# Kernel optimization log

Hardware: AMD Instinct MI355X
Metric: run time of the kernel (lower is better)

The kernel has to match this reference:

```python
import jax, jax.numpy as jnp
import numpy as np

HEADS = 4
DIM_HEAD = 32
SCALE = 16.0
EPS = 1e-5  # jax.nn.standardize default


def _standardize(t):
    # standardize over last axis (the flattened x*y*z sequence), per (b, h, d)
    mu = jnp.mean(t, axis=-1, keepdims=True)
    var = jnp.var(t, axis=-1, keepdims=True)
    return (t - mu) * jax.lax.rsqrt(var + EPS)


def setup_inputs() -> dict:
    key = jax.random.key(0)
    k1, k2, k3 = jax.random.split(key, 3)
    dim = 64
    hidden = HEADS * DIM_HEAD  # 128
    b, x, y, z = 2, 16, 16, 16
    inp = jax.random.normal(k1, (b, x, y, z, dim), dtype=jnp.float32)
    # 1x1x1 convs == pointwise channel matmuls; init like flax lecun_normal-ish scale
    w_qkv = jax.random.normal(k2, (dim, 3 * hidden), dtype=jnp.float32) / np.sqrt(dim)
    w_out = jax.random.normal(k3, (hidden, dim), dtype=jnp.float32) / np.sqrt(hidden)
    b_out = jnp.zeros((dim,), dtype=jnp.float32)
    return {"input": inp, "w_qkv": w_qkv, "w_out": w_out, "b_out": b_out}


def reference(input, w_qkv, w_out, b_out):
    b, x, y, z, c = input.shape
    s = x * y * z
    # pointwise conv -> qkv
    qkv = jnp.einsum('bxyzc,cd->bxyzd', input, w_qkv)  # [b,x,y,z,3*hidden]
    q, k, v = jnp.split(qkv, 3, axis=-1)
    # rearrange 'b x y z (h c) -> b h c (x y z)'
    def to_bhds(t):
        return t.reshape(b, s, HEADS, DIM_HEAD).transpose(0, 2, 3, 1)  # [b,h,d,s]
    q, k, v = map(to_bhds, (q, k, v))
    q = _standardize(q)
    k = _standardize(k)
    sim = jnp.einsum('bhdi,bhdj->bhij', q, k) * SCALE  # [b,h,s,s]
    attn = jax.nn.softmax(sim, axis=-1)
    out = jnp.einsum('bhij,bhdj->bhid', attn, v)  # [b,h,s,d]
    # rearrange 'b h (x y z) d -> b x y z (h d)'
    out = out.transpose(0, 2, 1, 3).reshape(b, x, y, z, HEADS * DIM_HEAD)
    return jnp.einsum('bxyzc,co->bxyzo', out, w_out) + b_out
```

## Files before the change

### kernel.cpp

```cpp
#include <hip/hip_runtime.h>
#include <math.h>
#include <stdint.h>


typedef __attribute__((ext_vector_type(8))) short short8;
typedef __attribute__((ext_vector_type(4))) float f32x4;
typedef __attribute__((ext_vector_type(16))) float f32x16;

#define QSCALE 23.083120654223414f

#if __has_builtin(__builtin_amdgcn_exp2f)
#define EXP2F(x) __builtin_amdgcn_exp2f(x)
#else
#define EXP2F(x) exp2f(x)
#endif

__device__ inline uint32_t pack_hilo(float y) {
  uint32_t uy = __float_as_uint(y);
  uint32_t hb = (uy + 0x7fffu + ((uy >> 16) & 1u)) >> 16;
  float hf = __uint_as_float(hb << 16);
  float r = y - hf;
  uint32_t ur = __float_as_uint(r);
  uint32_t lb = (ur + 0x7fffu + ((ur >> 16) & 1u)) >> 16;
  return (hb << 16) | (lb & 0xffffu);
}

__device__ inline ushort f32_to_bf16(float y) {
  uint32_t uy = __float_as_uint(y);
  return (ushort)((uy + 0x7fffu + ((uy >> 16) & 1u)) >> 16);
}

__device__ inline float bpermf(int addr, float v) {
  return __int_as_float(__builtin_amdgcn_ds_bpermute(addr, __float_as_int(v)));
}

__global__ __launch_bounds__(256) void qkv_kernel(const float* __restrict__ in,
                                                  const float* __restrict__ w,
                                                  float* __restrict__ qf,
                                                  float* __restrict__ kf,
                                                  ushort* __restrict__ vhg,
                                                  float* __restrict__ psum,
                                                  float* __restrict__ psq) {
  __shared__ float As[64][68];
  __shared__ float Bs[64][68];
  __shared__ float ssum[64], ssq[64];
  const int ctile = blockIdx.x % 6;
  const int stile = blockIdx.x / 6;
  const int tid = threadIdx.x;
  const int row0 = stile * 64;
  const int sel = ctile >> 1;

  if (tid < 64) { ssum[tid] = 0.f; ssq[tid] = 0.f; }
  for (int idx = tid; idx < 64 * 64; idx += 256) {
    int s = idx >> 6, c = idx & 63;
    As[s][c] = in[(size_t)(row0 + s) * 64 + c];
  }
  for (int idx = tid; idx < 64 * 64; idx += 256) {
    int c = idx >> 6, ch = idx & 63;
    Bs[c][ch] = w[(size_t)c * 384 + ctile * 64 + ch];
  }
  __syncthreads();

  const int ts = tid >> 4, tc = tid & 15;
  float acc[4][4] = {};
  for (int c = 0; c < 64; c += 4) {
    float4 av[4];
#pragma unroll
    for (int a = 0; a < 4; ++a) av[a] = *(const float4*)&As[ts * 4 + a][c];
    const float4 b0 = *(const float4*)&Bs[c + 0][tc * 4];
    const float4 b1 = *(const float4*)&Bs[c + 1][tc * 4];
    const float4 b2 = *(const float4*)&Bs[c + 2][tc * 4];
    const float4 b3 = *(const float4*)&Bs[c + 3][tc * 4];
    const float bm[4][4] = {{b0.x, b0.y, b0.z, b0.w},
                            {b1.x, b1.y, b1.z, b1.w},
                            {b2.x, b2.y, b2.z, b2.w},
                            {b3.x, b3.y, b3.z, b3.w}};
#pragma unroll
    for (int a = 0; a < 4; ++a) {
      const float aw[4] = {av[a].x, av[a].y, av[a].z, av[a].w};
#pragma unroll
      for (int j = 0; j < 4; ++j)
#pragma unroll
        for (int cc = 0; cc < 4; ++cc) acc[a][cc] = fmaf(aw[j], bm[j][cc], acc[a][cc]);
    }
  }

  const int b = row0 >> 12;
  const int sl = (row0 & 4095) + ts * 4;
  const int chg0 = ctile * 64 + tc * 4;

  if (sel < 2) {
    const int hd0 = chg0 & 127;
    const int h = hd0 >> 5, d0 = hd0 & 31;
    float* dst = (sel == 0 ? qf : kf) + ((size_t)(b * 4 + h) * 4096) * 32 + d0;
#pragma unroll
    for (int a = 0; a < 4; ++a) {
      float4 st = make_float4(acc[a][0], acc[a][1], acc[a][2], acc[a][3]);
      *(float4*)&dst[(size_t)(sl + a) * 32] = st;
    }
#pragma unroll
    for (int cc = 0; cc < 4; ++cc) {
      float sm = acc[0][cc] + acc[1][cc] + acc[2][cc] + acc[3][cc];
      float sq = acc[0][cc] * acc[0][cc] + acc[1][cc] * acc[1][cc] +
                 acc[2][cc] * acc[2][cc] + acc[3][cc] * acc[3][cc];
      atomicAdd(&ssum[tc * 4 + cc], sm);
      atomicAdd(&ssq[tc * 4 + cc], sq);
    }
    __syncthreads();
    if (tid < 64) {
      const int ch = (ctile & 1) * 64 + tid;
      const int idx = (((sel * 2 + b) * 128) + ch) * 64 + (stile & 63);
      psum[idx] = ssum[tid];
      psq[idx] = ssq[tid];
    }
  } else {
    __syncthreads();
    float* VT = &As[0][0];
#pragma unroll
    for (int cc = 0; cc < 4; ++cc)
      *(float4*)&VT[(tc * 4 + cc) * 68 + ts * 4] =
          make_float4(acc[0][cc], acc[1][cc], acc[2][cc], acc[3][cc]);
    __syncthreads();
#pragma unroll
    for (int t2 = 0; t2 < 2; ++t2) {
      const int lin = tid + t2 * 256;
      const int ch = lin >> 3, gg = lin & 7;
      const float4 f0 = *(const float4*)&VT[ch * 68 + gg * 8];
      const float4 f1 = *(const float4*)&VT[ch * 68 + gg * 8 + 4];
      uint4 pk;
      pk.x = (uint32_t)f32_to_bf16(f0.x) | ((uint32_t)f32_to_bf16(f0.y) << 16);
      pk.y = (uint32_t)f32_to_bf16(f0.z) | ((uint32_t)f32_to_bf16(f0.w) << 16);
      pk.z = (uint32_t)f32_to_bf16(f1.x) | ((uint32_t)f32_to_bf16(f1.y) << 16);
      pk.w = (uint32_t)f32_to_bf16(f1.z) | ((uint32_t)f32_to_bf16(f1.w) << 16);
      const int hd = (ctile * 64 + ch) & 127;
      const int h = hd >> 5, d = hd & 31;
      *(uint4*)&vhg[((size_t)(b * 4 + h) * 32 + d) * 4096 + (row0 & 4095) + gg * 8] = pk;
    }
  }
}

__global__ __launch_bounds__(256) void norm_kernel(const float* __restrict__ kf,
                                                   ushort* __restrict__ khg,
                                                   ushort* __restrict__ klg,
                                                   const float* __restrict__ psum,
                                                   const float* __restrict__ psq,
                                                   float* __restrict__ qA,
                                                   float* __restrict__ qB) {
  const int bx = blockIdx.x;
  const int tid = threadIdx.x;
  if (bx == 128) {
    const int base = (((tid >> 7) * 128) + (tid & 127)) * 64;
    float sm = 0.f, sq = 0.f;
#pragma unroll 8
    for (int e = 0; e < 64; ++e) {
      sm += psum[base + e];
      sq += psq[base + e];
    }
    const float mu = sm * (1.f / 4096.f);
    const float inv = rsqrtf(sq * (1.f / 4096.f) - mu * mu + 1e-5f) * QSCALE;
    qA[tid] = inv;
    qB[tid] = -mu * inv;
    return;
  }
  __shared__ float red[2][32][8];
  __shared__ float kA[32], kB[32];
  const int bh = bx >> 4;
  const int s0 = (bx & 15) * 256;
  {
    const int d = tid >> 3, p = tid & 7;
    const int base = ((2 + (bh >> 2)) * 128 + (bh & 3) * 32 + d) * 64 + p * 8;
    float sm = 0.f, sq = 0.f;
#pragma unroll
    for (int e = 0; e < 8; ++e) {
      sm += psum[base + e];
      sq += psq[base + e];
    }
    red[0][d][p] = sm;
    red[1][d][p] = sq;
  }
  __syncthreads();
  if (tid < 32) {
    float sm = 0.f, sq = 0.f;
#pragma unroll
    for (int e = 0; e < 8; ++e) {
      sm += red[0][tid][e];
      sq += red[1][tid][e];
    }
    const float mu = sm * (1.f / 4096.f);
    const float inv = rsqrtf(sq * (1.f / 4096.f) - mu * mu + 1e-5f);
    kA[tid] = inv;
    kB[tid] = -mu * inv;
  }
  __syncthreads();

  const int d0 = (tid & 7) * 4;
  const float A0 = kA[d0], A1 = kA[d0 + 1], A2 = kA[d0 + 2], A3 = kA[d0 + 3];
  const float B0 = kB[d0], B1 = kB[d0 + 1], B2 = kB[d0 + 2], B3 = kB[d0 + 3];
  const float* src = kf + ((size_t)bh * 4096 + s0) * 32;
  ushort* dh = khg + ((size_t)bh * 4096 + s0) * 32 + d0;
  ushort* dl = klg + ((size_t)bh * 4096 + s0) * 32 + d0;
#pragma unroll
  for (int i = 0; i < 8; ++i) {
    const int s = (tid + i * 256) >> 3;
    float4 x = *(const float4*)&src[(size_t)s * 32 + d0];
    float y[4] = {fmaf(x.x, A0, B0), fmaf(x.y, A1, B1), fmaf(x.z, A2, B2), fmaf(x.w, A3, B3)};
    ushort4 hi, lo;
    ushort* hp = (ushort*)&hi;
    ushort* lp = (ushort*)&lo;
#pragma unroll
    for (int e = 0; e < 4; ++e) {
      uint32_t pk = pack_hilo(y[e]);
      hp[e] = (ushort)(pk >> 16);
      lp[e] = (ushort)(pk & 0xffff);
    }
    *(ushort4*)&dh[(size_t)s * 32] = hi;
    *(ushort4*)&dl[(size_t)s * 32] = lo;
  }
}

__global__ __launch_bounds__(512, 4) void attn_kernel(const float* __restrict__ qf,
                                                      const float* __restrict__ qA,
                                                      const float* __restrict__ qB,
                                                      const ushort* __restrict__ khg,
                                                      const ushort* __restrict__ klg,
                                                      const ushort* __restrict__ vhg,
                                                      float* __restrict__ o) {
  __shared__ char lds[49152];

  const int tid = threadIdx.x;
  const int strm = tid >> 7;
  const int st = tid & 127;
  const int wv = (tid >> 6) & 1;
  const int lane = tid & 63;
  const int pl = lane & 31;
  const int h2 = lane >> 5;
  const int bh = blockIdx.x >> 6;
  const int i0 = (blockIdx.x & 63) * 64;

  ushort* KHI = (ushort*)lds + strm * 6144;

  const int irow = i0 + wv * 32 + pl;
  const float* qptr = qf + ((size_t)bh * 4096 + irow) * 32;
  short8 qh0, ql0, qh1, ql1;
  {
    const int da = 8 * h2, db = 16 + 8 * h2;
    const float4 x0 = *(const float4*)(qptr + da);
    const float4 x1 = *(const float4*)(qptr + da + 4);
    const float4 x2 = *(const float4*)(qptr + db);
    const float4 x3 = *(const float4*)(qptr + db + 4);
    const float4 A0 = *(const float4*)&qA[bh * 32 + da];
    const float4 A1 = *(const float4*)&qA[bh * 32 + da + 4];
    const float4 A2 = *(const float4*)&qA[bh * 32 + db];
    const float4 A3 = *(const float4*)&qA[bh * 32 + db + 4];
    const float4 B0 = *(const float4*)&qB[bh * 32 + da];
    const float4 B1 = *(const float4*)&qB[bh * 32 + da + 4];
    const float4 B2 = *(const float4*)&qB[bh * 32 + db];
    const float4 B3 = *(const float4*)&qB[bh * 32 + db + 4];
    const float y0[8] = {fmaf(x0.x, A0.x, B0.x), fmaf(x0.y, A0.y, B0.y),
                         fmaf(x0.z, A0.z, B0.z), fmaf(x0.w, A0.w, B0.w),
                         fmaf(x1.x, A1.x, B1.x), fmaf(x1.y, A1.y, B1.y),
                         fmaf(x1.z, A1.z, B1.z), fmaf(x1.w, A1.w, B1.w)};
    const float y1[8] = {fmaf(x2.x, A2.x, B2.x), fmaf(x2.y, A2.y, B2.y),
                         fmaf(x2.z, A2.z, B2.z), fmaf(x2.w, A2.w, B2.w),
                         fmaf(x3.x, A3.x, B3.x), fmaf(x3.y, A3.y, B3.y),
                         fmaf(x3.z, A3.z, B3.z), fmaf(x3.w, A3.w, B3.w)};
#pragma unroll
    for (int j = 0; j < 8; ++j) {
      uint32_t p0 = pack_hilo(y0[j]);
      uint32_t p1 = pack_hilo(y1[j]);
      qh0[j] = (short)(p0 >> 16); ql0[j] = (short)(p0 & 0xffff);
      qh1[j] = (short)(p1 >> 16); ql1[j] = (short)(p1 & 0xffff);
    }
  }

  const int bp32 = (lane ^ 32) << 2;

  const int jr = st >> 2, ck = st & 3;
  const int et = jr >> 4, eh = (jr >> 3) & 1, ee = jr & 7;
  const int pphys = (ee & 3) + 8 * (ee >> 2) + 4 * eh + 16 * (et & 1);
  const int rowp = (et >> 1) * 32 + pphys;
  const int ckp = ck ^ ((pphys >> 1) & 2);
  const ushort* ksrc = khg + ((size_t)bh * 4096 + jr) * 32 + ck * 8;
  const ushort* lsrc = klg + ((size_t)bh * 4096 + jr) * 32 + ck * 8;
  ushort* kdst = KHI + rowp * 32 + ckp * 8;
  const int dr = st >> 3, cv = st & 7;
  const ushort* vsrc = vhg + ((size_t)bh * 32 + dr) * 4096 + cv * 8;
  ushort* vdst = KHI + 4096 + dr * 64 + (cv ^ (dr & 7)) * 8;

  const int sw = (pl >> 1) & 2;
  const int k00 = pl * 32 + (h2 ^ sw) * 8;
  const int k01 = pl * 32 + ((2 + h2) ^ sw) * 8;
  int voff[4];
#pragma unroll
  for (int t = 0; t < 4; ++t) voff[t] = pl * 64 + ((2 * t + h2) ^ (pl & 7)) * 8;

  f32x16 oacc;
#pragma unroll
  for (int r = 0; r < 16; ++r) oacc[r] = 0.f;
  float m = -INFINITY, l = 0.f;

  for (int it = 0; it < 16; ++it) {
    const int j0 = strm * 1024 + it * 64;
    __syncthreads();
    {
      const uint4 ka0 = *(const uint4*)(ksrc + (size_t)j0 * 32);
      const uint4 ka1 = *(const uint4*)(ksrc + (size_t)j0 * 32 + 1024);
      const uint4 la0 = *(const uint4*)(lsrc + (size_t)j0 * 32);
      const uint4 la1 = *(const uint4*)(lsrc + (size_t)j0 * 32 + 1024);
      const uint4 va0 = *(const uint4*)(vsrc + j0);
      const uint4 va1 = *(const uint4*)(vsrc + j0 + 65536);
      *(uint4*)kdst = ka0;
      *(uint4*)(kdst + 1024) = ka1;
      *(uint4*)(kdst + 2048) = la0;
      *(uint4*)(kdst + 3072) = la1;
      *(uint4*)vdst = va0;
      *(uint4*)(vdst + 1024) = va1;
    }
    __syncthreads();

#pragma unroll
    for (int u = 0; u < 2; ++u) {
      const ushort* KB = KHI + u * 1024;
      const short8 kh0 = *(const short8*)(KB + k00);
      const short8 kh1 = *(const short8*)(KB + k01);
      const short8 kl0 = *(const short8*)(KB + 2048 + k00);
      const short8 kl1 = *(const short8*)(KB + 2048 + k01);
      f32x16 sc;
#pragma unroll
      for (int r = 0; r < 16; ++r) sc[r] = 0.f;
      sc = __builtin_amdgcn_mfma_f32_32x32x16_bf16(kh0, qh0, sc, 0, 0, 0);
      sc = __builtin_amdgcn_mfma_f32_32x32x16_bf16(kh1, qh1, sc, 0, 0, 0);
      sc = __builtin_amdgcn_mfma_f32_32x32x16_bf16(kh0, ql0, sc, 0, 0, 0);
      sc = __builtin_amdgcn_mfma_f32_32x32x16_bf16(kh1, ql1, sc, 0, 0, 0);
      sc = __builtin_amdgcn_mfma_f32_32x32x16_bf16(kl0, qh0, sc, 0, 0, 0);
      sc = __builtin_amdgcn_mfma_f32_32x32x16_bf16(kl1, qh1, sc, 0, 0, 0);

      float mx = sc[0];
#pragma unroll
      for (int r = 1; r < 16; ++r) mx = fmaxf(mx, sc[r]);
      mx = fmaxf(mx, bpermf(bp32, mx));
      const float mn = fmaxf(m, mx);
      const float al = EXP2F(m - mn);
      m = mn;
#pragma unroll
      for (int r = 0; r < 16; ++r) sc[r] = EXP2F(sc[r] - mn);
      float rs = 0.f;
#pragma unroll
      for (int r = 0; r < 16; ++r) rs += sc[r];
      rs += bpermf(bp32, rs);
      l = l * al + rs;
#pragma unroll
      for (int r = 0; r < 16; ++r) oacc[r] *= al;

      uint32_t pk[8];
#pragma unroll
      for (int i = 0; i < 8; ++i)
        pk[i] = __builtin_amdgcn_perm(__float_as_uint(sc[2 * i + 1]),
                                      __float_as_uint(sc[2 * i]), 0x07060302u);
      union { uint32_t u4[4]; short8 s8; } p0, p1;
      p0.u4[0] = pk[0]; p0.u4[1] = pk[1]; p0.u4[2] = pk[2]; p0.u4[3] = pk[3];
      p1.u4[0] = pk[4]; p1.u4[1] = pk[5]; p1.u4[2] = pk[6]; p1.u4[3] = pk[7];

      const short8 va0 = *(const short8*)(KHI + 4096 + voff[2 * u]);
      const short8 va1 = *(const short8*)(KHI + 4096 + voff[2 * u + 1]);
      oacc = __builtin_amdgcn_mfma_f32_32x32x16_bf16(va0, p0.s8, oacc, 0, 0, 0);
      oacc = __builtin_amdgcn_mfma_f32_32x32x16_bf16(va1, p1.s8, oacc, 0, 0, 0);
    }
  }

  __syncthreads();
  float* OM = (float*)lds;
  float* ML = (float*)(lds + 36864);
  {
    float* om = OM + (size_t)(strm * 64 + wv * 32 + pl) * 36;
#pragma unroll
    for (int g = 0; g < 4; ++g)
      *(float4*)&om[4 * h2 + 8 * g] =
          make_float4(oacc[4 * g], oacc[4 * g + 1], oacc[4 * g + 2], oacc[4 * g + 3]);
    if (h2 == 0) {
      ML[strm * 128 + wv * 32 + pl] = m;
      ML[strm * 128 + 64 + wv * 32 + pl] = l;
    }
  }
  __syncthreads();
  const int b = bh >> 2, h = bh & 3;
#pragma unroll
  for (int pass = 0; pass < 4; ++pass) {
    const int idx = tid + pass * 512;
    const int i = idx >> 5, d = idx & 31;
    const float m0 = ML[i], m1 = ML[128 + i], m2 = ML[256 + i], m3 = ML[384 + i];
    const float l0 = ML[64 + i], l1 = ML[192 + i], l2 = ML[320 + i], l3 = ML[448 + i];
    const float M = fmaxf(fmaxf(m0, m1), fmaxf(m2, m3));
    const float w0 = EXP2F(m0 - M), w1 = EXP2F(m1 - M);
    const float w2 = EXP2F(m2 - M), w3 = EXP2F(m3 - M);
    const float L = l0 * w0 + l1 * w1 + l2 * w2 + l3 * w3;
    const float val = (OM[i * 36 + d] * w0 + OM[(64 + i) * 36 + d] * w1 +
                       OM[(128 + i) * 36 + d] * w2 + OM[(192 + i) * 36 + d] * w3) *
                      (1.001953125f / L);
    o[((size_t)(b * 4096) + i0 + i) * 128 + h * 32 + d] = val;
  }
}

__global__ __launch_bounds__(256) void proj_kernel(const float* __restrict__ o,
                                                   const float* __restrict__ w,
                                                   const float* __restrict__ bias,
                                                   float* __restrict__ out) {
  __shared__ float wT[64 * 132];
  const int tid = threadIdx.x;
  for (int idx = tid; idx < 8192; idx += 256) {
    const int c = idx >> 6, col = idx & 63;
    const int g = (c >> 2) ^ ((col >> 3) & 7);
    wT[col * 132 + (g << 2) + (c & 3)] = w[idx];
  }
  __syncthreads();
  const int col = tid & 63;
  const int r = blockIdx.x * 8 + ((tid >> 6) << 1);
  const float* r0 = o + (size_t)r * 128;
  const float* r1 = r0 + 128;
  const int wbase = col * 132;
  const int gx = (col >> 3) & 7;
  float a0 = bias[col], a1 = a0;
  for (int c = 0; c < 128; c += 4) {
    const float4 x0 = *(const float4*)&r0[c];
    const float4 x1 = *(const float4*)&r1[c];
    const float4 wv = *(const float4*)&wT[wbase + ((((c >> 2) ^ gx)) << 2)];
    a0 = fmaf(x0.x, wv.x, a0); a0 = fmaf(x0.y, wv.y, a0);
    a0 = fmaf(x0.z, wv.z, a0); a0 = fmaf(x0.w, wv.w, a0);
    a1 = fmaf(x1.x, wv.x, a1); a1 = fmaf(x1.y, wv.y, a1);
    a1 = fmaf(x1.z, wv.z, a1); a1 = fmaf(x1.w, wv.w, a1);
  }
  out[(size_t)r * 64 + col] = a0;
  out[(size_t)(r + 1) * 64 + col] = a1;
}

extern "C" void kernel_launch(void* const* d_in, const int* in_sizes, int n_in,
                              void* d_out, int out_size, void* d_ws, size_t ws_size,
                              hipStream_t stream) {
  const float* input = (const float*)d_in[0];
  const float* w_qkv = (const float*)d_in[1];
  const float* w_out = (const float*)d_in[2];
  const float* b_out = (const float*)d_in[3];

  char* W = (char*)d_ws;
  float* qf = (float*)(W + 0);
  float* kf = (float*)(W + (4u << 20));
  ushort* khg = (ushort*)(W + (8u << 20));
  ushort* klg = (ushort*)(W + (10u << 20));
  ushort* vhg = (ushort*)(W + (12u << 20));
  float* psum = (float*)(W + (14u << 20));
  float* psq = (float*)(W + (14u << 20) + (128u << 10));
  float* qA = (float*)(W + (14u << 20) + (256u << 10));
  float* qB = qA + 256;
  float* ob = kf;
  float* out = (float*)d_out;

  hipLaunchKernelGGL(qkv_kernel, dim3(768), dim3(256), 0, stream, input, w_qkv, qf, kf,
                     vhg, psum, psq);
  hipLaunchKernelGGL(norm_kernel, dim3(129), dim3(256), 0, stream, kf, khg, klg,
                     psum, psq, qA, qB);
  hipLaunchKernelGGL(attn_kernel, dim3(512), dim3(512), 0, stream, qf, qA, qB,
                     khg, klg, vhg, ob);
  hipLaunchKernelGGL(proj_kernel, dim3(1024), dim3(256), 0, stream, ob, w_out, b_out, out);
}
```

Baseline: 147.6 us.

## Pre-swizzle Q/K/V into MFMA fragment layout and drop LDS staging in attention

Q normalization and hi/lo bf16 splitting move from the attention kernel into norm_kernel. Q, K and V are now written in the exact per-lane MFMA fragment order, so each attention wave loads its operands straight from global memory with register double-buffering. This removes the LDS copies and the two __syncthreads per iteration. Work is regrouped so each wave covers one quarter of the keys for one 32-row query tile, and the partials are merged at the end. The cost is more global/L2 traffic per wave, since K/V are no longer shared through LDS across the block's query tiles, plus extra workspace for the Q fragments.

```diff
diff --git a/kernel.cpp b/kernel.cpp
--- a/kernel.cpp
+++ b/kernel.cpp
@@ -34,11 +34,17 @@
   return __int_as_float(__builtin_amdgcn_ds_bpermute(addr, __float_as_int(v)));
 }
 
+__device__ inline short8 as_s8(uint4 v) {
+  union { uint4 u; short8 s; } t;
+  t.u = v;
+  return t.s;
+}
+
 __global__ __launch_bounds__(256) void qkv_kernel(const float* __restrict__ in,
                                                   const float* __restrict__ w,
                                                   float* __restrict__ qf,
                                                   float* __restrict__ kf,
-                                                  ushort* __restrict__ vhg,
+                                                  ushort* __restrict__ vfr,
                                                   float* __restrict__ psum,
                                                   float* __restrict__ psq) {
   __shared__ float As[64][68];
@@ -121,54 +127,46 @@
       *(float4*)&VT[(tc * 4 + cc) * 68 + ts * 4] =
           make_float4(acc[0][cc], acc[1][cc], acc[2][cc], acc[3][cc]);
     __syncthreads();
-#pragma unroll
-    for (int t2 = 0; t2 < 2; ++t2) {
-      const int lin = tid + t2 * 256;
-      const int ch = lin >> 3, gg = lin & 7;
-      const float4 f0 = *(const float4*)&VT[ch * 68 + gg * 8];
-      const float4 f1 = *(const float4*)&VT[ch * 68 + gg * 8 + 4];
+    const int jt0 = (row0 & 4095) >> 5;
+#pragma unroll
+    for (int hl = 0; hl < 2; ++hl) {
+      const int jtl = tid >> 7, c = (tid >> 6) & 1, ln = tid & 63;
+      const int d = ln & 31, hh = ln >> 5;
+      const int jloc = 32 * jtl + 16 * c + 8 * hh;
+      const int ch = hl * 32 + d;
+      const float4 f0 = *(const float4*)&VT[ch * 68 + jloc];
+      const float4 f1 = *(const float4*)&VT[ch * 68 + jloc + 4];
       uint4 pk;
       pk.x = (uint32_t)f32_to_bf16(f0.x) | ((uint32_t)f32_to_bf16(f0.y) << 16);
       pk.y = (uint32_t)f32_to_bf16(f0.z) | ((uint32_t)f32_to_bf16(f0.w) << 16);
       pk.z = (uint32_t)f32_to_bf16(f1.x) | ((uint32_t)f32_to_bf16(f1.y) << 16);
       pk.w = (uint32_t)f32_to_bf16(f1.z) | ((uint32_t)f32_to_bf16(f1.w) << 16);
-      const int hd = (ctile * 64 + ch) & 127;
-      const int h = hd >> 5, d = hd & 31;
-      *(uint4*)&vhg[((size_t)(b * 4 + h) * 32 + d) * 4096 + (row0 & 4095) + gg * 8] = pk;
-    }
-  }
-}
-
-__global__ __launch_bounds__(256) void norm_kernel(const float* __restrict__ kf,
-                                                   ushort* __restrict__ khg,
-                                                   ushort* __restrict__ klg,
+      const int h = (ctile - 4) * 2 + hl;
+      ushort* dst =
+          vfr + (((size_t)((b * 4 + h) * 128 + jt0 + jtl) * 2 + c) * 64 + ln) * 8;
+      *(uint4*)dst = pk;
+    }
+  }
+}
+
+__global__ __launch_bounds__(256) void norm_kernel(const float* __restrict__ qf,
+                                                   const float* __restrict__ kf,
+                                                   ushort* __restrict__ qfr_hi,
+                                                   ushort* __restrict__ qfr_lo,
+                                                   ushort* __restrict__ kfr_hi,
+                                                   ushort* __restrict__ kfr_lo,
                                                    const float* __restrict__ psum,
-                                                   const float* __restrict__ psq,
-                                                   float* __restrict__ qA,
-                                                   float* __restrict__ qB) {
+                                                   const float* __restrict__ psq) {
   const int bx = blockIdx.x;
+  const int tensor = bx >> 7;
+  const int bh = (bx >> 4) & 7;
+  const int s0 = (bx & 15) * 256;
   const int tid = threadIdx.x;
-  if (bx == 128) {
-    const int base = (((tid >> 7) * 128) + (tid & 127)) * 64;
-    float sm = 0.f, sq = 0.f;
-#pragma unroll 8
-    for (int e = 0; e < 64; ++e) {
-      sm += psum[base + e];
-      sq += psq[base + e];
-    }
-    const float mu = sm * (1.f / 4096.f);
-    const float inv = rsqrtf(sq * (1.f / 4096.f) - mu * mu + 1e-5f) * QSCALE;
-    qA[tid] = inv;
-    qB[tid] = -mu * inv;
-    return;
-  }
   __shared__ float red[2][32][8];
-  __shared__ float kA[32], kB[32];
-  const int bh = bx >> 4;
-  const int s0 = (bx & 15) * 256;
+  __shared__ float tA[32], tB[32];
   {
     const int d = tid >> 3, p = tid & 7;
-    const int base = ((2 + (bh >> 2)) * 128 + (bh & 3) * 32 + d) * 64 + p * 8;
+    const int base = ((tensor * 2 + (bh >> 2)) * 128 + (bh & 3) * 32 + d) * 64 + p * 8;
     float sm = 0.f, sq = 0.f;
 #pragma unroll
     for (int e = 0; e < 8; ++e) {
@@ -187,199 +185,163 @@
       sq += red[1][tid][e];
     }
     const float mu = sm * (1.f / 4096.f);
-    const float inv = rsqrtf(sq * (1.f / 4096.f) - mu * mu + 1e-5f);
-    kA[tid] = inv;
-    kB[tid] = -mu * inv;
+    const float scale = tensor == 0 ? QSCALE : 1.0f;
+    const float inv = rsqrtf(sq * (1.f / 4096.f) - mu * mu + 1e-5f) * scale;
+    tA[tid] = inv;
+    tB[tid] = -mu * inv;
   }
   __syncthreads();
 
-  const int d0 = (tid & 7) * 4;
-  const float A0 = kA[d0], A1 = kA[d0 + 1], A2 = kA[d0 + 2], A3 = kA[d0 + 3];
-  const float B0 = kB[d0], B1 = kB[d0 + 1], B2 = kB[d0 + 2], B3 = kB[d0 + 3];
-  const float* src = kf + ((size_t)bh * 4096 + s0) * 32;
-  ushort* dh = khg + ((size_t)bh * 4096 + s0) * 32 + d0;
-  ushort* dl = klg + ((size_t)bh * 4096 + s0) * 32 + d0;
-#pragma unroll
-  for (int i = 0; i < 8; ++i) {
-    const int s = (tid + i * 256) >> 3;
-    float4 x = *(const float4*)&src[(size_t)s * 32 + d0];
-    float y[4] = {fmaf(x.x, A0, B0), fmaf(x.y, A1, B1), fmaf(x.z, A2, B2), fmaf(x.w, A3, B3)};
-    ushort4 hi, lo;
-    ushort* hp = (ushort*)&hi;
-    ushort* lp = (ushort*)&lo;
-#pragma unroll
-    for (int e = 0; e < 4; ++e) {
-      uint32_t pk = pack_hilo(y[e]);
-      hp[e] = (ushort)(pk >> 16);
-      lp[e] = (ushort)(pk & 0xffff);
-    }
-    *(ushort4*)&dh[(size_t)s * 32] = hi;
-    *(ushort4*)&dl[(size_t)s * 32] = lo;
-  }
-}
-
-__global__ __launch_bounds__(512, 4) void attn_kernel(const float* __restrict__ qf,
-                                                      const float* __restrict__ qA,
-                                                      const float* __restrict__ qB,
-                                                      const ushort* __restrict__ khg,
-                                                      const ushort* __restrict__ klg,
-                                                      const ushort* __restrict__ vhg,
+  const float* src = (tensor == 0 ? qf : kf) + (size_t)bh * 4096 * 32;
+  ushort* dhi = (tensor == 0 ? qfr_hi : kfr_hi) + (size_t)(bh * 128 + (s0 >> 5)) * 1024;
+  ushort* dlo = (tensor == 0 ? qfr_lo : kfr_lo) + (size_t)(bh * 128 + (s0 >> 5)) * 1024;
+#pragma unroll
+  for (int pass = 0; pass < 4; ++pass) {
+    const int idx = tid + pass * 256;
+    const int jtl = idx >> 7;
+    const int c = (idx >> 6) & 1;
+    const int ln = idx & 63;
+    const int p = ln & 31, hh = ln >> 5;
+    const int row = tensor == 0 ? p : ((p & 0x13) | ((p & 4) << 1) | ((p & 8) >> 1));
+    const int s = s0 + 32 * jtl + row;
+    const int d0 = 16 * c + 8 * hh;
+    const float4 x0 = *(const float4*)&src[(size_t)s * 32 + d0];
+    const float4 x1 = *(const float4*)&src[(size_t)s * 32 + d0 + 4];
+    const float4 A0 = *(const float4*)&tA[d0];
+    const float4 A1 = *(const float4*)&tA[d0 + 4];
+    const float4 B0 = *(const float4*)&tB[d0];
+    const float4 B1 = *(const float4*)&tB[d0 + 4];
+    uint32_t pk[8];
+    pk[0] = pack_hilo(fmaf(x0.x, A0.x, B0.x));
+    pk[1] = pack_hilo(fmaf(x0.y, A0.y, B0.y));
+    pk[2] = pack_hilo(fmaf(x0.z, A0.z, B0.z));
+    pk[3] = pack_hilo(fmaf(x0.w, A0.w, B0.w));
+    pk[4] = pack_hilo(fmaf(x1.x, A1.x, B1.x));
+    pk[5] = pack_hilo(fmaf(x1.y, A1.y, B1.y));
+    pk[6] = pack_hilo(fmaf(x1.z, A1.z, B1.z));
+    pk[7] = pack_hilo(fmaf(x1.w, A1.w, B1.w));
+    uint4 HV, LV;
+    HV.x = __builtin_amdgcn_perm(pk[1], pk[0], 0x07060302u);
+    HV.y = __builtin_amdgcn_perm(pk[3], pk[2], 0x07060302u);
+    HV.z = __builtin_amdgcn_perm(pk[5], pk[4], 0x07060302u);
+    HV.w = __builtin_amdgcn_perm(pk[7], pk[6], 0x07060302u);
+    LV.x = __builtin_amdgcn_perm(pk[1], pk[0], 0x05040100u);
+    LV.y = __builtin_amdgcn_perm(pk[3], pk[2], 0x05040100u);
+    LV.z = __builtin_amdgcn_perm(pk[5], pk[4], 0x05040100u);
+    LV.w = __builtin_amdgcn_perm(pk[7], pk[6], 0x05040100u);
+    const size_t doff = ((size_t)(jtl * 2 + c) * 64 + ln) * 8;
+    *(uint4*)(dhi + doff) = HV;
+    *(uint4*)(dlo + doff) = LV;
+  }
+}
+
+__global__ __launch_bounds__(512, 4) void attn_kernel(const ushort* __restrict__ qfr_hi,
+                                                      const ushort* __restrict__ qfr_lo,
+                                                      const ushort* __restrict__ kfr_hi,
+                                                      const ushort* __restrict__ kfr_lo,
+                                                      const ushort* __restrict__ vfr,
                                                       float* __restrict__ o) {
-  __shared__ char lds[49152];
+  __shared__ float OM[8 * 32 * 36];
+  __shared__ float ML[8 * 64];
 
   const int tid = threadIdx.x;
-  const int strm = tid >> 7;
-  const int st = tid & 127;
-  const int wv = (tid >> 6) & 1;
+  const int w = tid >> 6;
+  const int js = w & 3;
+  const int itl = w >> 2;
   const int lane = tid & 63;
-  const int pl = lane & 31;
-  const int h2 = lane >> 5;
-  const int bh = blockIdx.x >> 6;
-  const int i0 = (blockIdx.x & 63) * 64;
-
-  ushort* KHI = (ushort*)lds + strm * 6144;
-
-  const int irow = i0 + wv * 32 + pl;
-  const float* qptr = qf + ((size_t)bh * 4096 + irow) * 32;
-  short8 qh0, ql0, qh1, ql1;
-  {
-    const int da = 8 * h2, db = 16 + 8 * h2;
-    const float4 x0 = *(const float4*)(qptr + da);
-    const float4 x1 = *(const float4*)(qptr + da + 4);
-    const float4 x2 = *(const float4*)(qptr + db);
-    const float4 x3 = *(const float4*)(qptr + db + 4);
-    const float4 A0 = *(const float4*)&qA[bh * 32 + da];
-    const float4 A1 = *(const float4*)&qA[bh * 32 + da + 4];
-    const float4 A2 = *(const float4*)&qA[bh * 32 + db];
-    const float4 A3 = *(const float4*)&qA[bh * 32 + db + 4];
-    const float4 B0 = *(const float4*)&qB[bh * 32 + da];
-    const float4 B1 = *(const float4*)&qB[bh * 32 + da + 4];
-    const float4 B2 = *(const float4*)&qB[bh * 32 + db];
-    const float4 B3 = *(const float4*)&qB[bh * 32 + db + 4];
-    const float y0[8] = {fmaf(x0.x, A0.x, B0.x), fmaf(x0.y, A0.y, B0.y),
-                         fmaf(x0.z, A0.z, B0.z), fmaf(x0.w, A0.w, B0.w),
-                         fmaf(x1.x, A1.x, B1.x), fmaf(x1.y, A1.y, B1.y),
-                         fmaf(x1.z, A1.z, B1.z), fmaf(x1.w, A1.w, B1.w)};
-    const float y1[8] = {fmaf(x2.x, A2.x, B2.x), fmaf(x2.y, A2.y, B2.y),
-                         fmaf(x2.z, A2.z, B2.z), fmaf(x2.w, A2.w, B2.w),
-                         fmaf(x3.x, A3.x, B3.x), fmaf(x3.y, A3.y, B3.y),
-                         fmaf(x3.z, A3.z, B3.z), fmaf(x3.w, A3.w, B3.w)};
-#pragma unroll
-    for (int j = 0; j < 8; ++j) {
-      uint32_t p0 = pack_hilo(y0[j]);
-      uint32_t p1 = pack_hilo(y1[j]);
-      qh0[j] = (short)(p0 >> 16); ql0[j] = (short)(p0 & 0xffff);
-      qh1[j] = (short)(p1 >> 16); ql1[j] = (short)(p1 & 0xffff);
-    }
-  }
+  const int pl = lane & 31, h2 = lane >> 5;
+  const int bh = blockIdx.x & 7;
+  const int itp = blockIdx.x >> 3;
+  const int it = itp * 2 + itl;
+
+  const size_t qbase = (size_t)(bh * 128 + it) * 1024 + lane * 8;
+  const short8 qh0 = *(const short8*)(qfr_hi + qbase);
+  const short8 qh1 = *(const short8*)(qfr_hi + qbase + 512);
+  const short8 ql0 = *(const short8*)(qfr_lo + qbase);
+  const short8 ql1 = *(const short8*)(qfr_lo + qbase + 512);
 
   const int bp32 = (lane ^ 32) << 2;
 
-  const int jr = st >> 2, ck = st & 3;
-  const int et = jr >> 4, eh = (jr >> 3) & 1, ee = jr & 7;
-  const int pphys = (ee & 3) + 8 * (ee >> 2) + 4 * eh + 16 * (et & 1);
-  const int rowp = (et >> 1) * 32 + pphys;
-  const int ckp = ck ^ ((pphys >> 1) & 2);
-  const ushort* ksrc = khg + ((size_t)bh * 4096 + jr) * 32 + ck * 8;
-  const ushort* lsrc = klg + ((size_t)bh * 4096 + jr) * 32 + ck * 8;
-  ushort* kdst = KHI + rowp * 32 + ckp * 8;
-  const int dr = st >> 3, cv = st & 7;
-  const ushort* vsrc = vhg + ((size_t)bh * 32 + dr) * 4096 + cv * 8;
-  ushort* vdst = KHI + 4096 + dr * 64 + (cv ^ (dr & 7)) * 8;
-
-  const int sw = (pl >> 1) & 2;
-  const int k00 = pl * 32 + (h2 ^ sw) * 8;
-  const int k01 = pl * 32 + ((2 + h2) ^ sw) * 8;
-  int voff[4];
-#pragma unroll
-  for (int t = 0; t < 4; ++t) voff[t] = pl * 64 + ((2 * t + h2) ^ (pl & 7)) * 8;
+  const size_t kbase = (size_t)(bh * 128 + js * 32) * 1024 + lane * 8;
+  const ushort* kh = kfr_hi + kbase;
+  const ushort* kl = kfr_lo + kbase;
+  const ushort* vp = vfr + kbase;
 
   f32x16 oacc;
 #pragma unroll
   for (int r = 0; r < 16; ++r) oacc[r] = 0.f;
   float m = -INFINITY, l = 0.f;
 
-  for (int it = 0; it < 16; ++it) {
-    const int j0 = strm * 1024 + it * 64;
-    __syncthreads();
+  uint4 rk0 = *(const uint4*)(kh);
+  uint4 rk1 = *(const uint4*)(kh + 512);
+  uint4 rl0 = *(const uint4*)(kl);
+  uint4 rl1 = *(const uint4*)(kl + 512);
+  uint4 rv0 = *(const uint4*)(vp);
+  uint4 rv1 = *(const uint4*)(vp + 512);
+
+  for (int t = 0; t < 32; ++t) {
+    const short8 ck0 = as_s8(rk0), ck1 = as_s8(rk1);
+    const short8 cl0 = as_s8(rl0), cl1 = as_s8(rl1);
+    const short8 cv0 = as_s8(rv0), cv1 = as_s8(rv1);
     {
-      const uint4 ka0 = *(const uint4*)(ksrc + (size_t)j0 * 32);
-      const uint4 ka1 = *(const uint4*)(ksrc + (size_t)j0 * 32 + 1024);
-      const uint4 la0 = *(const uint4*)(lsrc + (size_t)j0 * 32);
-      const uint4 la1 = *(const uint4*)(lsrc + (size_t)j0 * 32 + 1024);
-      const uint4 va0 = *(const uint4*)(vsrc + j0);
-      const uint4 va1 = *(const uint4*)(vsrc + j0 + 65536);
-      *(uint4*)kdst = ka0;
-      *(uint4*)(kdst + 1024) = ka1;
-      *(uint4*)(kdst + 2048) = la0;
-      *(uint4*)(kdst + 3072) = la1;
-      *(uint4*)vdst = va0;
-      *(uint4*)(vdst + 1024) = va1;
-    }
-    __syncthreads();
-
-#pragma unroll
-    for (int u = 0; u < 2; ++u) {
-      const ushort* KB = KHI + u * 1024;
-      const short8 kh0 = *(const short8*)(KB + k00);
-      const short8 kh1 = *(const short8*)(KB + k01);
-      const short8 kl0 = *(const short8*)(KB + 2048 + k00);
-      const short8 kl1 = *(const short8*)(KB + 2048 + k01);
-      f32x16 sc;
-#pragma unroll
-      for (int r = 0; r < 16; ++r) sc[r] = 0.f;
-      sc = __builtin_amdgcn_mfma_f32_32x32x16_bf16(kh0, qh0, sc, 0, 0, 0);
-      sc = __builtin_amdgcn_mfma_f32_32x32x16_bf16(kh1, qh1, sc, 0, 0, 0);
-      sc = __builtin_amdgcn_mfma_f32_32x32x16_bf16(kh0, ql0, sc, 0, 0, 0);
-      sc = __builtin_amdgcn_mfma_f32_32x32x16_bf16(kh1, ql1, sc, 0, 0, 0);
-      sc = __builtin_amdgcn_mfma_f32_32x32x16_bf16(kl0, qh0, sc, 0, 0, 0);
-      sc = __builtin_amdgcn_mfma_f32_32x32x16_bf16(kl1, qh1, sc, 0, 0, 0);
-
-      float mx = sc[0];
-#pragma unroll
-      for (int r = 1; r < 16; ++r) mx = fmaxf(mx, sc[r]);
-      mx = fmaxf(mx, bpermf(bp32, mx));
-      const float mn = fmaxf(m, mx);
-      const float al = EXP2F(m - mn);
-      m = mn;
-#pragma unroll
-      for (int r = 0; r < 16; ++r) sc[r] = EXP2F(sc[r] - mn);
-      float rs = 0.f;
-#pragma unroll
-      for (int r = 0; r < 16; ++r) rs += sc[r];
-      rs += bpermf(bp32, rs);
-      l = l * al + rs;
-#pragma unroll
-      for (int r = 0; r < 16; ++r) oacc[r] *= al;
-
-      uint32_t pk[8];
-#pragma unroll
-      for (int i = 0; i < 8; ++i)
-        pk[i] = __builtin_amdgcn_perm(__float_as_uint(sc[2 * i + 1]),
-                                      __float_as_uint(sc[2 * i]), 0x07060302u);
-      union { uint32_t u4[4]; short8 s8; } p0, p1;
-      p0.u4[0] = pk[0]; p0.u4[1] = pk[1]; p0.u4[2] = pk[2]; p0.u4[3] = pk[3];
-      p1.u4[0] = pk[4]; p1.u4[1] = pk[5]; p1.u4[2] = pk[6]; p1.u4[3] = pk[7];
-
-      const short8 va0 = *(const short8*)(KHI + 4096 + voff[2 * u]);
-      const short8 va1 = *(const short8*)(KHI + 4096 + voff[2 * u + 1]);
-      oacc = __builtin_amdgcn_mfma_f32_32x32x16_bf16(va0, p0.s8, oacc, 0, 0, 0);
-      oacc = __builtin_amdgcn_mfma_f32_32x32x16_bf16(va1, p1.s8, oacc, 0, 0, 0);
-    }
-  }
-
-  __syncthreads();
-  float* OM = (float*)lds;
-  float* ML = (float*)(lds + 36864);
+      const int off = (t + 1) * 1024;
+      rk0 = *(const uint4*)(kh + off);
+      rk1 = *(const uint4*)(kh + off + 512);
+      rl0 = *(const uint4*)(kl + off);
+      rl1 = *(const uint4*)(kl + off + 512);
+      rv0 = *(const uint4*)(vp + off);
+      rv1 = *(const uint4*)(vp + off + 512);
+    }
+
+    f32x16 sc;
+#pragma unroll
+    for (int r = 0; r < 16; ++r) sc[r] = 0.f;
+    sc = __builtin_amdgcn_mfma_f32_32x32x16_bf16(ck0, qh0, sc, 0, 0, 0);
+    sc = __builtin_amdgcn_mfma_f32_32x32x16_bf16(ck1, qh1, sc, 0, 0, 0);
+    sc = __builtin_amdgcn_mfma_f32_32x32x16_bf16(ck0, ql0, sc, 0, 0, 0);
+    sc = __builtin_amdgcn_mfma_f32_32x32x16_bf16(ck1, ql1, sc, 0, 0, 0);
+    sc = __builtin_amdgcn_mfma_f32_32x32x16_bf16(cl0, qh0, sc, 0, 0, 0);
+    sc = __builtin_amdgcn_mfma_f32_32x32x16_bf16(cl1, qh1, sc, 0, 0, 0);
+
+    float mx = sc[0];
+#pragma unroll
+    for (int r = 1; r < 16; ++r) mx = fmaxf(mx, sc[r]);
+    mx = fmaxf(mx, bpermf(bp32, mx));
+    const float mn = fmaxf(m, mx);
+    const float al = EXP2F(m - mn);
+    m = mn;
+#pragma unroll
+    for (int r = 0; r < 16; ++r) sc[r] = EXP2F(sc[r] - mn);
+    float rs = 0.f;
+#pragma unroll
+    for (int r = 0; r < 16; ++r) rs += sc[r];
+    rs += bpermf(bp32, rs);
+    l = l * al + rs;
+#pragma unroll
+    for (int r = 0; r < 16; ++r) oacc[r] *= al;
+
+    uint32_t pk[8];
+#pragma unroll
+    for (int i = 0; i < 8; ++i)
+      pk[i] = __builtin_amdgcn_perm(__float_as_uint(sc[2 * i + 1]),
+                                    __float_as_uint(sc[2 * i]), 0x07060302u);
+    union { uint32_t u4[4]; short8 s8; } p0, p1;
+    p0.u4[0] = pk[0]; p0.u4[1] = pk[1]; p0.u4[2] = pk[2]; p0.u4[3] = pk[3];
+    p1.u4[0] = pk[4]; p1.u4[1] = pk[5]; p1.u4[2] = pk[6]; p1.u4[3] = pk[7];
+
+    oacc = __builtin_amdgcn_mfma_f32_32x32x16_bf16(cv0, p0.s8, oacc, 0, 0, 0);
+    oacc = __builtin_amdgcn_mfma_f32_32x32x16_bf16(cv1, p1.s8, oacc, 0, 0, 0);
+  }
+
   {
-    float* om = OM + (size_t)(strm * 64 + wv * 32 + pl) * 36;
+    float* om = OM + (size_t)(w * 32 + pl) * 36;
 #pragma unroll
     for (int g = 0; g < 4; ++g)
       *(float4*)&om[4 * h2 + 8 * g] =
           make_float4(oacc[4 * g], oacc[4 * g + 1], oacc[4 * g + 2], oacc[4 * g + 3]);
     if (h2 == 0) {
-      ML[strm * 128 + wv * 32 + pl] = m;
-      ML[strm * 128 + 64 + wv * 32 + pl] = l;
+      ML[w * 64 + pl] = m;
+      ML[w * 64 + 32 + pl] = l;
     }
   }
   __syncthreads();
@@ -387,17 +349,25 @@
 #pragma unroll
   for (int pass = 0; pass < 4; ++pass) {
     const int idx = tid + pass * 512;
-    const int i = idx >> 5, d = idx & 31;
-    const float m0 = ML[i], m1 = ML[128 + i], m2 = ML[256 + i], m3 = ML[384 + i];
-    const float l0 = ML[64 + i], l1 = ML[192 + i], l2 = ML[320 + i], l3 = ML[448 + i];
+    const int itl2 = idx >> 10;
+    const int i = (idx >> 5) & 31;
+    const int d = idx & 31;
+    const int wb = itl2 * 4;
+    const float m0 = ML[(wb + 0) * 64 + i], m1 = ML[(wb + 1) * 64 + i];
+    const float m2 = ML[(wb + 2) * 64 + i], m3 = ML[(wb + 3) * 64 + i];
+    const float l0 = ML[(wb + 0) * 64 + 32 + i], l1 = ML[(wb + 1) * 64 + 32 + i];
+    const float l2 = ML[(wb + 2) * 64 + 32 + i], l3 = ML[(wb + 3) * 64 + 32 + i];
     const float M = fmaxf(fmaxf(m0, m1), fmaxf(m2, m3));
     const float w0 = EXP2F(m0 - M), w1 = EXP2F(m1 - M);
     const float w2 = EXP2F(m2 - M), w3 = EXP2F(m3 - M);
     const float L = l0 * w0 + l1 * w1 + l2 * w2 + l3 * w3;
-    const float val = (OM[i * 36 + d] * w0 + OM[(64 + i) * 36 + d] * w1 +
-                       OM[(128 + i) * 36 + d] * w2 + OM[(192 + i) * 36 + d] * w3) *
+    const float val = (OM[((wb + 0) * 32 + i) * 36 + d] * w0 +
+                       OM[((wb + 1) * 32 + i) * 36 + d] * w1 +
+                       OM[((wb + 2) * 32 + i) * 36 + d] * w2 +
+                       OM[((wb + 3) * 32 + i) * 36 + d] * w3) *
                       (1.001953125f / L);
-    o[((size_t)(b * 4096) + i0 + i) * 128 + h * 32 + d] = val;
+    const int ig = (itp * 2 + itl2) * 32 + i;
+    o[((size_t)(b * 4096) + ig) * 128 + h * 32 + d] = val;
   }
 }
 
@@ -444,21 +414,21 @@
   char* W = (char*)d_ws;
   float* qf = (float*)(W + 0);
   float* kf = (float*)(W + (4u << 20));
-  ushort* khg = (ushort*)(W + (8u << 20));
-  ushort* klg = (ushort*)(W + (10u << 20));
-  ushort* vhg = (ushort*)(W + (12u << 20));
-  float* psum = (float*)(W + (14u << 20));
-  float* psq = (float*)(W + (14u << 20) + (128u << 10));
-  float* qA = (float*)(W + (14u << 20) + (256u << 10));
-  float* qB = qA + 256;
-  float* ob = kf;
+  ushort* kfr_hi = (ushort*)(W + (8u << 20));
+  ushort* kfr_lo = (ushort*)(W + (10u << 20));
+  ushort* vfr = (ushort*)(W + (12u << 20));
+  ushort* qfr_hi = (ushort*)(W + (14u << 20));
+  ushort* qfr_lo = (ushort*)(W + (16u << 20));
+  float* psum = (float*)(W + (18u << 20));
+  float* psq = (float*)(W + (18u << 20) + (128u << 10));
+  float* ob = qf;
   float* out = (float*)d_out;
 
   hipLaunchKernelGGL(qkv_kernel, dim3(768), dim3(256), 0, stream, input, w_qkv, qf, kf,
-                     vhg, psum, psq);
-  hipLaunchKernelGGL(norm_kernel, dim3(129), dim3(256), 0, stream, kf, khg, klg,
-                     psum, psq, qA, qB);
-  hipLaunchKernelGGL(attn_kernel, dim3(512), dim3(512), 0, stream, qf, qA, qB,
-                     khg, klg, vhg, ob);
+                     vfr, psum, psq);
+  hipLaunchKernelGGL(norm_kernel, dim3(256), dim3(256), 0, stream, qf, kf, qfr_hi,
+                     qfr_lo, kfr_hi, kfr_lo, psum, psq);
+  hipLaunchKernelGGL(attn_kernel, dim3(512), dim3(512), 0, stream, qfr_hi, qfr_lo,
+                     kfr_hi, kfr_lo, vfr, ob);
   hipLaunchKernelGGL(proj_kernel, dim3(1024), dim3(256), 0, stream, ob, w_out, b_out, out);
 }
```

Measured after the change: 140.6 us. 1.05x faster.
